# Kernel tuning notes

Hardware: AMD Instinct MI355X
Metric: run time of the kernel (lower is better)

## Reference

```python
import jax, jax.numpy as jnp
import numpy as np

B, L, D = 2, 2048, 1024
H, DH = 16, 64
HIDDEN = 4096
DILATION, WINDOW, CAUSAL = 2, 512, True
EPS = 1e-5


def _ln(x, g, b):
    m = jnp.mean(x, axis=-1, keepdims=True)
    v = jnp.mean(jnp.square(x - m), axis=-1, keepdims=True)
    return (x - m) * jax.lax.rsqrt(v + EPS) * g + b


def setup_inputs() -> dict:
    key = jax.random.key(0)
    ks = jax.random.split(key, 8)
    s = 0.02
    return {
        "x": jax.random.normal(ks[0], (B, L, D), jnp.float32),
        "ln1_g": jnp.ones((D,), jnp.float32),
        "ln1_b": jnp.zeros((D,), jnp.float32),
        "w_qkv": jax.random.normal(ks[1], (3 * D, D), jnp.float32) * s,
        "b_qkv": jnp.zeros((3 * D,), jnp.float32),
        "w_o": jax.random.normal(ks[2], (D, D), jnp.float32) * s,
        "b_o": jnp.zeros((D,), jnp.float32),
        "ln2_g": jnp.ones((D,), jnp.float32),
        "ln2_b": jnp.zeros((D,), jnp.float32),
        "w_ff1": jax.random.normal(ks[3], (HIDDEN, D), jnp.float32) * s,
        "b_ff1": jnp.zeros((HIDDEN,), jnp.float32),
        "w_ff2": jax.random.normal(ks[4], (D, HIDDEN), jnp.float32) * s,
        "b_ff2": jnp.zeros((D,), jnp.float32),
    }


def reference(x, ln1_g, ln1_b, w_qkv, b_qkv, w_o, b_o, ln2_g, ln2_b, w_ff1, b_ff1, w_ff2, b_ff2):
    # pre-norm attention block with dilated/windowed/causal mask
    h = _ln(x, ln1_g, ln1_b)
    qkv = h @ w_qkv.T + b_qkv                      # [B, L, 3D]
    q, k, v = jnp.split(qkv, 3, axis=-1)
    q = q.reshape(B, L, H, DH)
    k = k.reshape(B, L, H, DH)
    v = v.reshape(B, L, H, DH)

    scale = 1.0 / jnp.sqrt(jnp.float32(DH))
    scores = jnp.einsum("bqhd,bkhd->bhqk", q, k) * scale  # [B, H, L, L]

    i = jnp.arange(L)[:, None]
    j = jnp.arange(L)[None, :]
    allowed = ((i - j) % DILATION == 0) & (jnp.abs(i - j) <= WINDOW)
    if CAUSAL:
        allowed = allowed & (j <= i)
    scores = jnp.where(allowed, scores, -jnp.inf)  # diagonal always allowed -> rows finite

    p = jax.nn.softmax(scores, axis=-1)
    attn = jnp.einsum("bhqk,bkhd->bqhd", p, v).reshape(B, L, D)

    out = x + attn @ w_o.T + b_o                   # residual 1 (dropout p=0)

    h2 = _ln(out, ln2_g, ln2_b)
    ff = jax.nn.gelu(h2 @ w_ff1.T + b_ff1, approximate=False) @ w_ff2.T + b_ff2
    return out + ff                                # residual 2
```

## Files before the change

kernel.cpp:

```cpp
#include <hip/hip_runtime.h>
#include <hip/hip_bf16.h>
#include <cmath>

#define Bsz 2
#define Lseq 2048
#define Dmod 1024
#define Hhead 16
#define DH 64
#define HID 4096
#define ROWS (Bsz * Lseq)
#define TD (3 * Dmod)

typedef __attribute__((ext_vector_type(8))) short bf16x8;
typedef __attribute__((ext_vector_type(4))) float f32x4;
typedef unsigned short ushort_t;

typedef const __attribute__((address_space(1))) void gv_t;
typedef __attribute__((address_space(3))) void lv_t;
#define GLDS16(GP, LP) __builtin_amdgcn_global_load_lds((gv_t*)(GP), (lv_t*)(LP), 16, 0, 0)

__device__ __forceinline__ float bf2f(short u)
{
    return __uint_as_float(((unsigned)(unsigned short)u) << 16);
}
__device__ __forceinline__ unsigned pack2(float a, float b)
{
    __hip_bfloat162 t;
    t.x = __float2bfloat16(a);
    t.y = __float2bfloat16(b);
    return *reinterpret_cast<unsigned*>(&t);
}
__device__ __forceinline__ float gelu_exact(float t)
{
    return 0.5f * t * (1.0f + erff(t * 0.70710678118654752f));
}

__device__ __forceinline__ void xcd_remap(int& mblk, int& nblk)
{
    int nx = gridDim.x;
    int nwg = nx * gridDim.y;
    int id = blockIdx.y * nx + blockIdx.x;
    int cpx = nwg >> 3;
    int swz = (id & 7) * cpx + (id >> 3);
    mblk = swz / nx;
    nblk = swz % nx;
}

__global__ __launch_bounds__(256) void f2b4_kernel(const float* __restrict__ s0, ushort_t* __restrict__ d0,
                                                   const float* __restrict__ s1, ushort_t* __restrict__ d1,
                                                   const float* __restrict__ s2, ushort_t* __restrict__ d2,
                                                   const float* __restrict__ s3, ushort_t* __restrict__ d3)
{
    int blk = blockIdx.x;
    const float* src;
    ushort_t* dst;
    int base;
    if (blk < 3072)      { src = s0; dst = d0; base = blk; }
    else if (blk < 4096) { src = s1; dst = d1; base = blk - 3072; }
    else if (blk < 8192) { src = s2; dst = d2; base = blk - 4096; }
    else                 { src = s3; dst = d3; base = blk - 8192; }
    int i = base * 256 + threadIdx.x;
    float4 v = reinterpret_cast<const float4*>(src)[i];
    uint2 o;
    o.x = pack2(v.x, v.y);
    o.y = pack2(v.z, v.w);
    reinterpret_cast<uint2*>(dst)[i] = o;
}

__global__ __launch_bounds__(256) void ln_kernel(const float* __restrict__ x,
                                                 const float* __restrict__ g,
                                                 const float* __restrict__ bta,
                                                 ushort_t* __restrict__ out)
{
    int row = blockIdx.x;
    int t = threadIdx.x;
    const float4* xr = reinterpret_cast<const float4*>(x) + (size_t)row * 256;
    float4 v = xr[t];
    float s  = v.x + v.y + v.z + v.w;
    float s2 = v.x * v.x + v.y * v.y + v.z * v.z + v.w * v.w;
#pragma unroll
    for (int o = 32; o > 0; o >>= 1) {
        s  += __shfl_down(s, o);
        s2 += __shfl_down(s2, o);
    }
    __shared__ float sa[4], sb[4];
    int wv = t >> 6, ln = t & 63;
    if (ln == 0) { sa[wv] = s; sb[wv] = s2; }
    __syncthreads();
    s  = sa[0] + sa[1] + sa[2] + sa[3];
    s2 = sb[0] + sb[1] + sb[2] + sb[3];
    float mean = s * (1.0f / 1024.0f);
    float var  = s2 * (1.0f / 1024.0f) - mean * mean;
    float inv  = rsqrtf(var + 1e-5f);
    float4 gv = reinterpret_cast<const float4*>(g)[t];
    float4 bv = reinterpret_cast<const float4*>(bta)[t];
    uint2 o;
    o.x = pack2((v.x - mean) * inv * gv.x + bv.x, (v.y - mean) * inv * gv.y + bv.y);
    o.y = pack2((v.z - mean) * inv * gv.z + bv.z, (v.w - mean) * inv * gv.w + bv.w);
    reinterpret_cast<uint2*>(out)[(size_t)row * 256 + t] = o;
}

__global__ __launch_bounds__(256) void gemm_bt(const ushort_t* __restrict__ A,
                                               const ushort_t* __restrict__ W,
                                               const float* __restrict__ bias,
                                               const float* __restrict__ res,
                                               void* __restrict__ C,
                                               int M, int N, int K, int ldw,
                                               int act, int obf)
{
    __shared__ ushort_t As0[128 * 64];
    __shared__ ushort_t Bs0[128 * 64];
    __shared__ ushort_t As1[128 * 64];
    __shared__ ushort_t Bs1[128 * 64];

    int tid = threadIdx.x;
    int w = tid >> 6, lane = tid & 63;
    int mblk, nblk;
    xcd_remap(mblk, nblk);
    int m0 = mblk * 128, n0 = nblk * 128;
    int wr = (w >> 1) * 64, wc = (w & 1) * 64;

    int srow = lane >> 3;
    int scol = (((lane & 7) ^ (lane >> 3)) & 7) * 8;
    const ushort_t* ga[4];
    const ushort_t* gb[4];
    int lofs[4];
#pragma unroll
    for (int q = 0; q < 4; ++q) {
        ga[q] = A + (size_t)(m0 + w * 32 + q * 8 + srow) * K + scol;
        gb[q] = W + (size_t)(n0 + w * 32 + q * 8 + srow) * ldw + scol;
        lofs[q] = (w * 32 + q * 8) * 64;
    }

    int fr = lane & 15;
    int fg = lane >> 4;
    int r0 = fg * 4;
    int cc = fr;

    f32x4 acc[4][4] = {};

    auto stage = [&](ushort_t* AS, ushort_t* BS, int k0) {
#pragma unroll
        for (int q = 0; q < 4; ++q) {
            GLDS16(ga[q] + k0, AS + lofs[q]);
            GLDS16(gb[q] + k0, BS + lofs[q]);
        }
    };
    auto compute = [&](const ushort_t* AS, const ushort_t* BS) {
#pragma unroll
        for (int kk = 0; kk < 2; ++kk) {
            bf16x8 af[4], bfr[4];
            int ca = ((kk * 4 + fg) ^ (fr & 7)) * 8;
#pragma unroll
            for (int i = 0; i < 4; ++i) {
                af[i]  = *reinterpret_cast<const bf16x8*>(&AS[(wr + i * 16 + fr) * 64 + ca]);
                bfr[i] = *reinterpret_cast<const bf16x8*>(&BS[(wc + i * 16 + fr) * 64 + ca]);
            }
#pragma unroll
            for (int mi = 0; mi < 4; ++mi)
#pragma unroll
                for (int ni = 0; ni < 4; ++ni)
                    acc[mi][ni] = __builtin_amdgcn_mfma_f32_16x16x32_bf16(
                        af[mi], bfr[ni], acc[mi][ni], 0, 0, 0);
        }
    };

    int nt = K >> 6;
    stage(As0, Bs0, 0);
    stage(As1, Bs1, 64);
    int t = 0;
    for (; t + 3 < nt; t += 2) {
        asm volatile("s_waitcnt vmcnt(8)" ::: "memory");
        __builtin_amdgcn_s_barrier();
        __builtin_amdgcn_sched_barrier(0);
        compute(As0, Bs0);
        __builtin_amdgcn_s_barrier();
        stage(As0, Bs0, (t + 2) * 64);

        asm volatile("s_waitcnt vmcnt(8)" ::: "memory");
        __builtin_amdgcn_s_barrier();
        __builtin_amdgcn_sched_barrier(0);
        compute(As1, Bs1);
        __builtin_amdgcn_s_barrier();
        stage(As1, Bs1, (t + 3) * 64);
    }
    asm volatile("s_waitcnt vmcnt(8)" ::: "memory");
    __builtin_amdgcn_s_barrier();
    __builtin_amdgcn_sched_barrier(0);
    compute(As0, Bs0);
    asm volatile("s_waitcnt vmcnt(0)" ::: "memory");
    __builtin_amdgcn_s_barrier();
    __builtin_amdgcn_sched_barrier(0);
    compute(As1, Bs1);

    float bv[4];
#pragma unroll
    for (int ni = 0; ni < 4; ++ni)
        bv[ni] = bias ? bias[n0 + wc + ni * 16 + cc] : 0.0f;

#pragma unroll
    for (int mi = 0; mi < 4; ++mi) {
#pragma unroll
        for (int r = 0; r < 4; ++r) {
            int row = m0 + wr + mi * 16 + r0 + r;
            const float* resrow = res ? res + (size_t)row * N : nullptr;
#pragma unroll
            for (int ni = 0; ni < 4; ++ni) {
                int col = n0 + wc + ni * 16 + cc;
                float v = acc[mi][ni][r] + bv[ni];
                if (act == 1) v = gelu_exact(v);
                if (resrow) v += resrow[col];
                if (obf) {
                    reinterpret_cast<ushort_t*>(C)[(size_t)row * N + col] =
                        (ushort_t)__bfloat16_as_ushort(__float2bfloat16(v));
                } else {
                    reinterpret_cast<float*>(C)[(size_t)row * N + col] = v;
                }
            }
        }
    }
}

__global__ __launch_bounds__(256) void gemm_n64(const ushort_t* __restrict__ A,
                                                const ushort_t* __restrict__ W,
                                                const float* __restrict__ bias,
                                                const float* __restrict__ res,
                                                void* __restrict__ C,
                                                int M, int N, int K, int ldw,
                                                int act, int obf)
{
    __shared__ ushort_t As0[128 * 64];
    __shared__ ushort_t Bs0[64 * 64];
    __shared__ ushort_t As1[128 * 64];
    __shared__ ushort_t Bs1[64 * 64];

    int tid = threadIdx.x;
    int w = tid >> 6, lane = tid & 63;
    int mblk, nblk;
    xcd_remap(mblk, nblk);
    int m0 = mblk * 128, n0 = nblk * 64;
    int wr = (w >> 1) * 64, wc = (w & 1) * 32;

    int srow = lane >> 3;
    int scol = (((lane & 7) ^ (lane >> 3)) & 7) * 8;
    const ushort_t* ga[4];
    const ushort_t* gb[2];
    int laofs[4], lbofs[2];
#pragma unroll
    for (int q = 0; q < 4; ++q) {
        ga[q] = A + (size_t)(m0 + w * 32 + q * 8 + srow) * K + scol;
        laofs[q] = (w * 32 + q * 8) * 64;
    }
#pragma unroll
    for (int q = 0; q < 2; ++q) {
        gb[q] = W + (size_t)(n0 + w * 16 + q * 8 + srow) * ldw + scol;
        lbofs[q] = (w * 16 + q * 8) * 64;
    }

    int fr = lane & 15;
    int fg = lane >> 4;
    int r0 = fg * 4;
    int cc = fr;

    f32x4 acc[4][2] = {};

    auto stage = [&](ushort_t* AS, ushort_t* BS, int k0) {
#pragma unroll
        for (int q = 0; q < 4; ++q) GLDS16(ga[q] + k0, AS + laofs[q]);
#pragma unroll
        for (int q = 0; q < 2; ++q) GLDS16(gb[q] + k0, BS + lbofs[q]);
    };
    auto compute = [&](const ushort_t* AS, const ushort_t* BS) {
#pragma unroll
        for (int kk = 0; kk < 2; ++kk) {
            bf16x8 af[4], bfr[2];
            int ca = ((kk * 4 + fg) ^ (fr & 7)) * 8;
#pragma unroll
            for (int i = 0; i < 4; ++i)
                af[i] = *reinterpret_cast<const bf16x8*>(&AS[(wr + i * 16 + fr) * 64 + ca]);
#pragma unroll
            for (int i = 0; i < 2; ++i)
                bfr[i] = *reinterpret_cast<const bf16x8*>(&BS[(wc + i * 16 + fr) * 64 + ca]);
#pragma unroll
            for (int mi = 0; mi < 4; ++mi)
#pragma unroll
                for (int ni = 0; ni < 2; ++ni)
                    acc[mi][ni] = __builtin_amdgcn_mfma_f32_16x16x32_bf16(
                        af[mi], bfr[ni], acc[mi][ni], 0, 0, 0);
        }
    };

    int nt = K >> 6;
    stage(As0, Bs0, 0);
    stage(As1, Bs1, 64);
    int t = 0;
    for (; t + 3 < nt; t += 2) {
        asm volatile("s_waitcnt vmcnt(6)" ::: "memory");
        __builtin_amdgcn_s_barrier();
        __builtin_amdgcn_sched_barrier(0);
        compute(As0, Bs0);
        __builtin_amdgcn_s_barrier();
        stage(As0, Bs0, (t + 2) * 64);

        asm volatile("s_waitcnt vmcnt(6)" ::: "memory");
        __builtin_amdgcn_s_barrier();
        __builtin_amdgcn_sched_barrier(0);
        compute(As1, Bs1);
        __builtin_amdgcn_s_barrier();
        stage(As1, Bs1, (t + 3) * 64);
    }
    asm volatile("s_waitcnt vmcnt(6)" ::: "memory");
    __builtin_amdgcn_s_barrier();
    __builtin_amdgcn_sched_barrier(0);
    compute(As0, Bs0);
    asm volatile("s_waitcnt vmcnt(0)" ::: "memory");
    __builtin_amdgcn_s_barrier();
    __builtin_amdgcn_sched_barrier(0);
    compute(As1, Bs1);

    float bv[2];
#pragma unroll
    for (int ni = 0; ni < 2; ++ni)
        bv[ni] = bias ? bias[n0 + wc + ni * 16 + cc] : 0.0f;

#pragma unroll
    for (int mi = 0; mi < 4; ++mi) {
#pragma unroll
        for (int r = 0; r < 4; ++r) {
            int row = m0 + wr + mi * 16 + r0 + r;
            const float* resrow = res ? res + (size_t)row * N : nullptr;
#pragma unroll
            for (int ni = 0; ni < 2; ++ni) {
                int col = n0 + wc + ni * 16 + cc;
                float v = acc[mi][ni][r] + bv[ni];
                if (act == 1) v = gelu_exact(v);
                if (resrow) v += resrow[col];
                if (obf) {
                    reinterpret_cast<ushort_t*>(C)[(size_t)row * N + col] =
                        (ushort_t)__bfloat16_as_ushort(__float2bfloat16(v));
                } else {
                    reinterpret_cast<float*>(C)[(size_t)row * N + col] = v;
                }
            }
        }
    }
}

__global__ __launch_bounds__(256) void attn_mfma(const ushort_t* __restrict__ qkv,
                                                 ushort_t* __restrict__ out)
{
    __shared__ ushort_t Vt[64][328];
    __shared__ ushort_t Pw[4][16][40];

    int bid = blockIdx.x;
    int qt = bid & 15, h = (bid >> 4) & 15, p = (bid >> 8) & 1, b = bid >> 9;
    int qt0 = qt * 64;
    int kstart = qt0 - 256;

    const ushort_t* base = qkv + (size_t)b * Lseq * TD;
    int tid = threadIdx.x;

#pragma unroll
    for (int it = 0; it < 10; ++it) {
        int idx = it * 256 + tid;
        int ko = idx >> 3;
        int dg = idx & 7;
        int kk = kstart + ko;
        bf16x8 v = {};
        if (kk >= 0)
            v = *reinterpret_cast<const bf16x8*>(base + (size_t)(2 * kk + p) * TD + 2048 + h * 64 + dg * 8);
#pragma unroll
        for (int j = 0; j < 8; ++j)
            Vt[dg * 8 + j][ko] = (ushort_t)v[j];
    }

    int w = tid >> 6, lane = tid & 63;
    int fr = lane & 15, fg = lane >> 4;
    int qw = qt0 + w * 16;
    const ushort_t* qrow = base + (size_t)(2 * (qw + fr) + p) * TD + h * 64;
    bf16x8 qf0 = *reinterpret_cast<const bf16x8*>(qrow + fg * 8);
    bf16x8 qf1 = *reinterpret_cast<const bf16x8*>(qrow + 32 + fg * 8);

    __syncthreads();

    float m[4]    = {-1e30f, -1e30f, -1e30f, -1e30f};
    float lsum[4] = {};
    f32x4 o[4]    = {};
    const float scale = 0.125f;
    int qbase = qw + fg * 4;

    for (int t = 0; t < 10; ++t) {
        int kt0 = kstart + t * 32;
        int kk0 = kt0 + fr, kk1 = kk0 + 16;
        int kk0c = kk0 < 0 ? 0 : kk0;
        int kk1c = kk1 < 0 ? 0 : kk1;
        const ushort_t* kr0 = base + (size_t)(2 * kk0c + p) * TD + 1024 + h * 64;
        const ushort_t* kr1 = base + (size_t)(2 * kk1c + p) * TD + 1024 + h * 64;
        bf16x8 k00 = *reinterpret_cast<const bf16x8*>(kr0 + fg * 8);
        bf16x8 k01 = *reinterpret_cast<const bf16x8*>(kr0 + 32 + fg * 8);
        bf16x8 k10 = *reinterpret_cast<const bf16x8*>(kr1 + fg * 8);
        bf16x8 k11 = *reinterpret_cast<const bf16x8*>(kr1 + 32 + fg * 8);

        f32x4 s0 = {}, s1 = {};
        s0 = __builtin_amdgcn_mfma_f32_16x16x32_bf16(qf0, k00, s0, 0, 0, 0);
        s0 = __builtin_amdgcn_mfma_f32_16x16x32_bf16(qf1, k01, s0, 0, 0, 0);
        s1 = __builtin_amdgcn_mfma_f32_16x16x32_bf16(qf0, k10, s1, 0, 0, 0);
        s1 = __builtin_amdgcn_mfma_f32_16x16x32_bf16(qf1, k11, s1, 0, 0, 0);

        int c0 = kt0 + fr, c1 = c0 + 16;
        float v0[4], v1[4], tmax[4];
#pragma unroll
        for (int r = 0; r < 4; ++r) {
            int qq = qbase + r;
            bool a0 = (c0 >= 0) && (c0 <= qq) && (c0 >= qq - 256);
            bool a1 = (c1 >= 0) && (c1 <= qq) && (c1 >= qq - 256);
            v0[r] = a0 ? s0[r] * scale : -1e30f;
            v1[r] = a1 ? s1[r] * scale : -1e30f;
            tmax[r] = fmaxf(v0[r], v1[r]);
        }
#pragma unroll
        for (int off = 1; off < 16; off <<= 1) {
#pragma unroll
            for (int r = 0; r < 4; ++r)
                tmax[r] = fmaxf(tmax[r], __shfl_xor(tmax[r], off));
        }
#pragma unroll
        for (int r = 0; r < 4; ++r) {
            float mn = fmaxf(m[r], tmax[r]);
            float corr = __expf(m[r] - mn);
            m[r] = mn;
            float p0 = __expf(v0[r] - mn);
            float p1 = __expf(v1[r] - mn);
            lsum[r] = lsum[r] * corr + p0 + p1;
#pragma unroll
            for (int db = 0; db < 4; ++db)
                o[db][r] *= corr;
            Pw[w][fg * 4 + r][fr]      = (ushort_t)__bfloat16_as_ushort(__float2bfloat16(p0));
            Pw[w][fg * 4 + r][fr + 16] = (ushort_t)__bfloat16_as_ushort(__float2bfloat16(p1));
        }

        bf16x8 pf = *reinterpret_cast<const bf16x8*>(&Pw[w][fr][fg * 8]);
#pragma unroll
        for (int db = 0; db < 4; ++db) {
            bf16x8 vf = *reinterpret_cast<const bf16x8*>(&Vt[db * 16 + fr][t * 32 + fg * 8]);
            o[db] = __builtin_amdgcn_mfma_f32_16x16x32_bf16(pf, vf, o[db], 0, 0, 0);
        }
    }

#pragma unroll
    for (int off = 1; off < 16; off <<= 1) {
#pragma unroll
        for (int r = 0; r < 4; ++r)
            lsum[r] += __shfl_xor(lsum[r], off);
    }
    float inv[4];
#pragma unroll
    for (int r = 0; r < 4; ++r) inv[r] = 1.0f / lsum[r];

#pragma unroll
    for (int r = 0; r < 4; ++r) {
        size_t orow = ((size_t)b * Lseq + 2 * (qbase + r) + p) * Dmod + h * 64;
#pragma unroll
        for (int db = 0; db < 4; ++db)
            out[orow + db * 16 + fr] =
                (ushort_t)__bfloat16_as_ushort(__float2bfloat16(o[db][r] * inv[r]));
    }
}

extern "C" void kernel_launch(void* const* d_in, const int* in_sizes, int n_in,
                              void* d_out, int out_size, void* d_ws, size_t ws_size,
                              hipStream_t stream)
{
    const float* x     = (const float*)d_in[0];
    const float* ln1_g = (const float*)d_in[1];
    const float* ln1_b = (const float*)d_in[2];
    const float* w_qkv = (const float*)d_in[3];
    const float* b_qkv = (const float*)d_in[4];
    const float* w_o   = (const float*)d_in[5];
    const float* b_o   = (const float*)d_in[6];
    const float* ln2_g = (const float*)d_in[7];
    const float* ln2_b = (const float*)d_in[8];
    const float* w_ff1 = (const float*)d_in[9];
    const float* b_ff1 = (const float*)d_in[10];
    const float* w_ff2 = (const float*)d_in[11];
    const float* b_ff2 = (const float*)d_in[12];
    float* out = (float*)d_out;

    ushort_t* wq     = (ushort_t*)d_ws;
    ushort_t* wo     = wq  + (size_t)TD * Dmod;
    ushort_t* wf1    = wo  + (size_t)Dmod * Dmod;
    ushort_t* wf2    = wf1 + (size_t)HID * Dmod;
    ushort_t* bufFF  = wf2 + (size_t)Dmod * HID;
    ushort_t* bufH   = bufFF + (size_t)ROWS * HID;
    ushort_t* bufAtt = bufH + (size_t)ROWS * Dmod;

    f2b4_kernel<<<12288, 256, 0, stream>>>(w_qkv, wq, w_o, wo, w_ff1, wf1, w_ff2, wf2);

    ln_kernel<<<ROWS, 256, 0, stream>>>(x, ln1_g, ln1_b, bufH);
    gemm_bt<<<dim3(TD / 128, ROWS / 128), 256, 0, stream>>>(bufH, wq, b_qkv, nullptr,
                                                            bufFF, ROWS, TD, Dmod, Dmod, 0, 1);
    attn_mfma<<<Bsz * 2 * Hhead * (1024 / 64), 256, 0, stream>>>(bufFF, bufAtt);
    gemm_n64<<<dim3(Dmod / 64, ROWS / 128), 256, 0, stream>>>(bufAtt, wo, b_o, x,
                                                              out, ROWS, Dmod, Dmod, Dmod, 0, 0);
    ln_kernel<<<ROWS, 256, 0, stream>>>(out, ln2_g, ln2_b, bufH);
    gemm_bt<<<dim3(HID / 128, ROWS / 128), 256, 0, stream>>>(bufH, wf1, b_ff1, nullptr,
                                                             bufFF, ROWS, HID, Dmod, Dmod, 1, 1);
    gemm_n64<<<dim3(Dmod / 64, ROWS / 128), 256, 0, stream>>>(bufFF, wf2, b_ff2, out,
                                                              out, ROWS, Dmod, HID, HID, 0, 0);
}
```

Baseline: 236.0 us.

## Use 256x256 tiles with 8-wave blocks and prioritized MFMA phases for QKV/FF1 GEMMs

Replaces the 128x128, 4-wave GEMM with a 256x256, 8-wave kernel where each wave computes a 128x64 sub-tile. B fragments are preloaded per K-step and A fragments streamed in pairs, with s_setprio around MFMA bursts and barriers between phases. This raises arithmetic intensity and reduces global and LDS traffic per flop. In exchange it uses 128KB of LDS per block and produces far fewer blocks, which risks low CU occupancy and wave imbalance, especially for the QKV GEMM with 192 blocks.

New measurement: 241.2 us. 1.02x slower.

```diff
diff --git a/kernel.cpp b/kernel.cpp
--- a/kernel.cpp
+++ b/kernel.cpp
@@ -100,44 +100,45 @@
     reinterpret_cast<uint2*>(out)[(size_t)row * 256 + t] = o;
 }
 
-__global__ __launch_bounds__(256) void gemm_bt(const ushort_t* __restrict__ A,
-                                               const ushort_t* __restrict__ W,
-                                               const float* __restrict__ bias,
-                                               const float* __restrict__ res,
-                                               void* __restrict__ C,
-                                               int M, int N, int K, int ldw,
-                                               int act, int obf)
-{
-    __shared__ ushort_t As0[128 * 64];
-    __shared__ ushort_t Bs0[128 * 64];
-    __shared__ ushort_t As1[128 * 64];
-    __shared__ ushort_t Bs1[128 * 64];
+__global__ __launch_bounds__(512, 2) void gemm_256(const ushort_t* __restrict__ A,
+                                                   const ushort_t* __restrict__ W,
+                                                   const float* __restrict__ bias,
+                                                   const float* __restrict__ res,
+                                                   void* __restrict__ C,
+                                                   int M, int N, int K, int ldw,
+                                                   int act, int obf)
+{
+    __shared__ ushort_t As0[256 * 64];
+    __shared__ ushort_t Bs0[256 * 64];
+    __shared__ ushort_t As1[256 * 64];
+    __shared__ ushort_t Bs1[256 * 64];
 
     int tid = threadIdx.x;
     int w = tid >> 6, lane = tid & 63;
     int mblk, nblk;
     xcd_remap(mblk, nblk);
-    int m0 = mblk * 128, n0 = nblk * 128;
-    int wr = (w >> 1) * 64, wc = (w & 1) * 64;
+    int m0 = mblk * 256, n0 = nblk * 256;
+    int wr = (w >> 2) * 128;
+    int wc = (w & 3) * 64;
 
     int srow = lane >> 3;
-    int scol = (((lane & 7) ^ (lane >> 3)) & 7) * 8;
+    int scol = (((lane & 7) ^ srow) & 7) * 8;
     const ushort_t* ga[4];
     const ushort_t* gb[4];
     int lofs[4];
 #pragma unroll
     for (int q = 0; q < 4; ++q) {
-        ga[q] = A + (size_t)(m0 + w * 32 + q * 8 + srow) * K + scol;
-        gb[q] = W + (size_t)(n0 + w * 32 + q * 8 + srow) * ldw + scol;
-        lofs[q] = (w * 32 + q * 8) * 64;
+        int r = q * 64 + w * 8 + srow;
+        ga[q] = A + (size_t)(m0 + r) * K + scol;
+        gb[q] = W + (size_t)(n0 + r) * ldw + scol;
+        lofs[q] = r * 64;
     }
 
     int fr = lane & 15;
     int fg = lane >> 4;
     int r0 = fg * 4;
-    int cc = fr;
-
-    f32x4 acc[4][4] = {};
+
+    f32x4 acc[8][4] = {};
 
     auto stage = [&](ushort_t* AS, ushort_t* BS, int k0) {
 #pragma unroll
@@ -146,22 +147,38 @@
             GLDS16(gb[q] + k0, BS + lofs[q]);
         }
     };
-    auto compute = [&](const ushort_t* AS, const ushort_t* BS) {
-#pragma unroll
-        for (int kk = 0; kk < 2; ++kk) {
-            bf16x8 af[4], bfr[4];
-            int ca = ((kk * 4 + fg) ^ (fr & 7)) * 8;
-#pragma unroll
-            for (int i = 0; i < 4; ++i) {
-                af[i]  = *reinterpret_cast<const bf16x8*>(&AS[(wr + i * 16 + fr) * 64 + ca]);
-                bfr[i] = *reinterpret_cast<const bf16x8*>(&BS[(wc + i * 16 + fr) * 64 + ca]);
+
+    auto computeT = [&](const ushort_t* AS, const ushort_t* BS) {
+        bf16x8 bfr[4][2];
+#pragma unroll
+        for (int ni = 0; ni < 4; ++ni)
+#pragma unroll
+            for (int kk = 0; kk < 2; ++kk) {
+                int ca = ((kk * 4 + fg) ^ (fr & 7)) * 8;
+                bfr[ni][kk] = *reinterpret_cast<const bf16x8*>(&BS[(wc + ni * 16 + fr) * 64 + ca]);
             }
 #pragma unroll
-            for (int mi = 0; mi < 4; ++mi)
+        for (int p = 0; p < 4; ++p) {
+            bf16x8 af[2][2];
+#pragma unroll
+            for (int mi2 = 0; mi2 < 2; ++mi2)
+#pragma unroll
+                for (int kk = 0; kk < 2; ++kk) {
+                    int mi = p * 2 + mi2;
+                    int ca = ((kk * 4 + fg) ^ (fr & 7)) * 8;
+                    af[mi2][kk] = *reinterpret_cast<const bf16x8*>(&AS[(wr + mi * 16 + fr) * 64 + ca]);
+                }
+            __builtin_amdgcn_s_setprio(1);
+#pragma unroll
+            for (int mi2 = 0; mi2 < 2; ++mi2)
 #pragma unroll
                 for (int ni = 0; ni < 4; ++ni)
-                    acc[mi][ni] = __builtin_amdgcn_mfma_f32_16x16x32_bf16(
-                        af[mi], bfr[ni], acc[mi][ni], 0, 0, 0);
+#pragma unroll
+                    for (int kk = 0; kk < 2; ++kk)
+                        acc[p * 2 + mi2][ni] = __builtin_amdgcn_mfma_f32_16x16x32_bf16(
+                            af[mi2][kk], bfr[ni][kk], acc[p * 2 + mi2][ni], 0, 0, 0);
+            __builtin_amdgcn_s_setprio(0);
+            __builtin_amdgcn_s_barrier();
         }
     };
 
@@ -173,40 +190,40 @@
         asm volatile("s_waitcnt vmcnt(8)" ::: "memory");
         __builtin_amdgcn_s_barrier();
         __builtin_amdgcn_sched_barrier(0);
-        compute(As0, Bs0);
-        __builtin_amdgcn_s_barrier();
+        computeT(As0, Bs0);
+        __builtin_amdgcn_sched_barrier(0);
         stage(As0, Bs0, (t + 2) * 64);
 
         asm volatile("s_waitcnt vmcnt(8)" ::: "memory");
         __builtin_amdgcn_s_barrier();
         __builtin_amdgcn_sched_barrier(0);
-        compute(As1, Bs1);
-        __builtin_amdgcn_s_barrier();
+        computeT(As1, Bs1);
+        __builtin_amdgcn_sched_barrier(0);
         stage(As1, Bs1, (t + 3) * 64);
     }
     asm volatile("s_waitcnt vmcnt(8)" ::: "memory");
     __builtin_amdgcn_s_barrier();
     __builtin_amdgcn_sched_barrier(0);
-    compute(As0, Bs0);
+    computeT(As0, Bs0);
     asm volatile("s_waitcnt vmcnt(0)" ::: "memory");
     __builtin_amdgcn_s_barrier();
     __builtin_amdgcn_sched_barrier(0);
-    compute(As1, Bs1);
+    computeT(As1, Bs1);
 
     float bv[4];
 #pragma unroll
     for (int ni = 0; ni < 4; ++ni)
-        bv[ni] = bias ? bias[n0 + wc + ni * 16 + cc] : 0.0f;
-
-#pragma unroll
-    for (int mi = 0; mi < 4; ++mi) {
+        bv[ni] = bias ? bias[n0 + wc + ni * 16 + fr] : 0.0f;
+
+#pragma unroll
+    for (int mi = 0; mi < 8; ++mi) {
 #pragma unroll
         for (int r = 0; r < 4; ++r) {
             int row = m0 + wr + mi * 16 + r0 + r;
             const float* resrow = res ? res + (size_t)row * N : nullptr;
 #pragma unroll
             for (int ni = 0; ni < 4; ++ni) {
-                int col = n0 + wc + ni * 16 + cc;
+                int col = n0 + wc + ni * 16 + fr;
                 float v = acc[mi][ni][r] + bv[ni];
                 if (act == 1) v = gelu_exact(v);
                 if (resrow) v += resrow[col];
@@ -497,14 +514,14 @@
     f2b4_kernel<<<12288, 256, 0, stream>>>(w_qkv, wq, w_o, wo, w_ff1, wf1, w_ff2, wf2);
 
     ln_kernel<<<ROWS, 256, 0, stream>>>(x, ln1_g, ln1_b, bufH);
-    gemm_bt<<<dim3(TD / 128, ROWS / 128), 256, 0, stream>>>(bufH, wq, b_qkv, nullptr,
-                                                            bufFF, ROWS, TD, Dmod, Dmod, 0, 1);
+    gemm_256<<<dim3(TD / 256, ROWS / 256), 512, 0, stream>>>(bufH, wq, b_qkv, nullptr,
+                                                             bufFF, ROWS, TD, Dmod, Dmod, 0, 1);
     attn_mfma<<<Bsz * 2 * Hhead * (1024 / 64), 256, 0, stream>>>(bufFF, bufAtt);
     gemm_n64<<<dim3(Dmod / 64, ROWS / 128), 256, 0, stream>>>(bufAtt, wo, b_o, x,
                                                               out, ROWS, Dmod, Dmod, Dmod, 0, 0);
     ln_kernel<<<ROWS, 256, 0, stream>>>(out, ln2_g, ln2_b, bufH);
-    gemm_bt<<<dim3(HID / 128, ROWS / 128), 256, 0, stream>>>(bufH, wf1, b_ff1, nullptr,
-                                                             bufFF, ROWS, HID, Dmod, Dmod, 1, 1);
+    gemm_256<<<dim3(HID / 256, ROWS / 256), 512, 0, stream>>>(bufH, wf1, b_ff1, nullptr,
+                                                              bufFF, ROWS, HID, Dmod, Dmod, 1, 1);
     gemm_n64<<<dim3(Dmod / 64, ROWS / 128), 256, 0, stream>>>(bufFF, wf2, b_ff2, out,
                                                               out, ROWS, Dmod, HID, HID, 0, 0);
 }
```

## Give each wave private LDS tiles to drop block barriers in GEMM

Applied to the files above, without the earlier changes.

The QKV and FF1 GEMM kernel now has each wave stage its own 64x64 A and B sub-tiles into a private LDS region, so the workgroup-wide s_barrier calls around compute and staging are removed. Each wave loads twice as many global-to-LDS chunks, which duplicates A/B loads across waves and doubles global traffic per block. MFMA sections are wrapped in s_setprio, and launch bounds now request one block per CU. The aim is to remove barrier stalls at the cost of extra memory bandwidth and LDS footprint.

After: 294.0 us. +24.6%, slower.

```diff
diff --git a/kernel.cpp b/kernel.cpp
--- a/kernel.cpp
+++ b/kernel.cpp
@@ -100,36 +100,40 @@
     reinterpret_cast<uint2*>(out)[(size_t)row * 256 + t] = o;
 }
 
-__global__ __launch_bounds__(256) void gemm_bt(const ushort_t* __restrict__ A,
-                                               const ushort_t* __restrict__ W,
-                                               const float* __restrict__ bias,
-                                               const float* __restrict__ res,
-                                               void* __restrict__ C,
-                                               int M, int N, int K, int ldw,
-                                               int act, int obf)
-{
-    __shared__ ushort_t As0[128 * 64];
-    __shared__ ushort_t Bs0[128 * 64];
-    __shared__ ushort_t As1[128 * 64];
-    __shared__ ushort_t Bs1[128 * 64];
+__global__ __launch_bounds__(256, 1) void gemm_wp(const ushort_t* __restrict__ A,
+                                                  const ushort_t* __restrict__ W,
+                                                  const float* __restrict__ bias,
+                                                  const float* __restrict__ res,
+                                                  void* __restrict__ C,
+                                                  int M, int N, int K, int ldw,
+                                                  int act, int obf)
+{
+    __shared__ ushort_t As0[4 * 64 * 64];
+    __shared__ ushort_t Bs0[4 * 64 * 64];
+    __shared__ ushort_t As1[4 * 64 * 64];
+    __shared__ ushort_t Bs1[4 * 64 * 64];
 
     int tid = threadIdx.x;
     int w = tid >> 6, lane = tid & 63;
     int mblk, nblk;
     xcd_remap(mblk, nblk);
     int m0 = mblk * 128, n0 = nblk * 128;
-    int wr = (w >> 1) * 64, wc = (w & 1) * 64;
+    int wrb = (w >> 1) * 64;
+    int wcb = (w & 1) * 64;
+
+    ushort_t* a0 = As0 + w * 4096;
+    ushort_t* b0 = Bs0 + w * 4096;
+    ushort_t* a1 = As1 + w * 4096;
+    ushort_t* b1 = Bs1 + w * 4096;
 
     int srow = lane >> 3;
-    int scol = (((lane & 7) ^ (lane >> 3)) & 7) * 8;
-    const ushort_t* ga[4];
-    const ushort_t* gb[4];
-    int lofs[4];
-#pragma unroll
-    for (int q = 0; q < 4; ++q) {
-        ga[q] = A + (size_t)(m0 + w * 32 + q * 8 + srow) * K + scol;
-        gb[q] = W + (size_t)(n0 + w * 32 + q * 8 + srow) * ldw + scol;
-        lofs[q] = (w * 32 + q * 8) * 64;
+    int scol = (((lane & 7) ^ srow) & 7) * 8;
+    const ushort_t* ga[8];
+    const ushort_t* gb[8];
+#pragma unroll
+    for (int q = 0; q < 8; ++q) {
+        ga[q] = A + (size_t)(m0 + wrb + q * 8 + srow) * K + scol;
+        gb[q] = W + (size_t)(n0 + wcb + q * 8 + srow) * ldw + scol;
     }
 
     int fr = lane & 15;
@@ -141,9 +145,9 @@
 
     auto stage = [&](ushort_t* AS, ushort_t* BS, int k0) {
 #pragma unroll
-        for (int q = 0; q < 4; ++q) {
-            GLDS16(ga[q] + k0, AS + lofs[q]);
-            GLDS16(gb[q] + k0, BS + lofs[q]);
+        for (int q = 0; q < 8; ++q) {
+            GLDS16(ga[q] + k0, AS + q * 512);
+            GLDS16(gb[q] + k0, BS + q * 512);
         }
     };
     auto compute = [&](const ushort_t* AS, const ushort_t* BS) {
@@ -153,60 +157,58 @@
             int ca = ((kk * 4 + fg) ^ (fr & 7)) * 8;
 #pragma unroll
             for (int i = 0; i < 4; ++i) {
-                af[i]  = *reinterpret_cast<const bf16x8*>(&AS[(wr + i * 16 + fr) * 64 + ca]);
-                bfr[i] = *reinterpret_cast<const bf16x8*>(&BS[(wc + i * 16 + fr) * 64 + ca]);
+                af[i]  = *reinterpret_cast<const bf16x8*>(&AS[(i * 16 + fr) * 64 + ca]);
+                bfr[i] = *reinterpret_cast<const bf16x8*>(&BS[(i * 16 + fr) * 64 + ca]);
             }
+            __builtin_amdgcn_s_setprio(1);
 #pragma unroll
             for (int mi = 0; mi < 4; ++mi)
 #pragma unroll
                 for (int ni = 0; ni < 4; ++ni)
                     acc[mi][ni] = __builtin_amdgcn_mfma_f32_16x16x32_bf16(
                         af[mi], bfr[ni], acc[mi][ni], 0, 0, 0);
+            __builtin_amdgcn_s_setprio(0);
         }
     };
 
     int nt = K >> 6;
-    stage(As0, Bs0, 0);
-    stage(As1, Bs1, 64);
+    stage(a0, b0, 0);
+    stage(a1, b1, 64);
     int t = 0;
     for (; t + 3 < nt; t += 2) {
-        asm volatile("s_waitcnt vmcnt(8)" ::: "memory");
-        __builtin_amdgcn_s_barrier();
+        asm volatile("s_waitcnt vmcnt(16)" ::: "memory");
         __builtin_amdgcn_sched_barrier(0);
-        compute(As0, Bs0);
-        __builtin_amdgcn_s_barrier();
-        stage(As0, Bs0, (t + 2) * 64);
-
-        asm volatile("s_waitcnt vmcnt(8)" ::: "memory");
-        __builtin_amdgcn_s_barrier();
+        compute(a0, b0);
         __builtin_amdgcn_sched_barrier(0);
-        compute(As1, Bs1);
-        __builtin_amdgcn_s_barrier();
-        stage(As1, Bs1, (t + 3) * 64);
-    }
-    asm volatile("s_waitcnt vmcnt(8)" ::: "memory");
-    __builtin_amdgcn_s_barrier();
+        stage(a0, b0, (t + 2) * 64);
+
+        asm volatile("s_waitcnt vmcnt(16)" ::: "memory");
+        __builtin_amdgcn_sched_barrier(0);
+        compute(a1, b1);
+        __builtin_amdgcn_sched_barrier(0);
+        stage(a1, b1, (t + 3) * 64);
+    }
+    asm volatile("s_waitcnt vmcnt(16)" ::: "memory");
     __builtin_amdgcn_sched_barrier(0);
-    compute(As0, Bs0);
+    compute(a0, b0);
     asm volatile("s_waitcnt vmcnt(0)" ::: "memory");
-    __builtin_amdgcn_s_barrier();
     __builtin_amdgcn_sched_barrier(0);
-    compute(As1, Bs1);
+    compute(a1, b1);
 
     float bv[4];
 #pragma unroll
     for (int ni = 0; ni < 4; ++ni)
-        bv[ni] = bias ? bias[n0 + wc + ni * 16 + cc] : 0.0f;
+        bv[ni] = bias ? bias[n0 + wcb + ni * 16 + cc] : 0.0f;
 
 #pragma unroll
     for (int mi = 0; mi < 4; ++mi) {
 #pragma unroll
         for (int r = 0; r < 4; ++r) {
-            int row = m0 + wr + mi * 16 + r0 + r;
+            int row = m0 + wrb + mi * 16 + r0 + r;
             const float* resrow = res ? res + (size_t)row * N : nullptr;
 #pragma unroll
             for (int ni = 0; ni < 4; ++ni) {
-                int col = n0 + wc + ni * 16 + cc;
+                int col = n0 + wcb + ni * 16 + cc;
                 float v = acc[mi][ni][r] + bv[ni];
                 if (act == 1) v = gelu_exact(v);
                 if (resrow) v += resrow[col];
@@ -497,13 +499,13 @@
     f2b4_kernel<<<12288, 256, 0, stream>>>(w_qkv, wq, w_o, wo, w_ff1, wf1, w_ff2, wf2);
 
     ln_kernel<<<ROWS, 256, 0, stream>>>(x, ln1_g, ln1_b, bufH);
-    gemm_bt<<<dim3(TD / 128, ROWS / 128), 256, 0, stream>>>(bufH, wq, b_qkv, nullptr,
+    gemm_wp<<<dim3(TD / 128, ROWS / 128), 256, 0, stream>>>(bufH, wq, b_qkv, nullptr,
                                                             bufFF, ROWS, TD, Dmod, Dmod, 0, 1);
     attn_mfma<<<Bsz * 2 * Hhead * (1024 / 64), 256, 0, stream>>>(bufFF, bufAtt);
     gemm_n64<<<dim3(Dmod / 64, ROWS / 128), 256, 0, stream>>>(bufAtt, wo, b_o, x,
                                                               out, ROWS, Dmod, Dmod, Dmod, 0, 0);
     ln_kernel<<<ROWS, 256, 0, stream>>>(out, ln2_g, ln2_b, bufH);
-    gemm_bt<<<dim3(HID / 128, ROWS / 128), 256, 0, stream>>>(bufH, wf1, b_ff1, nullptr,
+    gemm_wp<<<dim3(HID / 128, ROWS / 128), 256, 0, stream>>>(bufH, wf1, b_ff1, nullptr,
                                                              bufFF, ROWS, HID, Dmod, Dmod, 1, 1);
     gemm_n64<<<dim3(Dmod / 64, ROWS / 128), 256, 0, stream>>>(bufFF, wf2, b_ff2, out,
                                                               out, ROWS, Dmod, HID, HID, 0, 0);
```
